# Kernel optimization log

Hardware: AMD Instinct MI355X
Metric: run time of the kernel (lower is better)

## Reference

```python
import jax, jax.numpy as jnp
import numpy as np

BLOCK_SIZE = 64
IN_CHANNELS = 1024
OUT_CHANNELS = 1024
O_NBLOCKS = OUT_CHANNELS // BLOCK_SIZE  # 16
I_NBLOCKS = IN_CHANNELS // BLOCK_SIZE   # 16
N_TOKENS = 32768


def setup_inputs() -> dict:
    key = jax.random.key(0)
    kx, kw = jax.random.split(key)
    x = jax.random.normal(kx, (N_TOKENS, IN_CHANNELS), dtype=jnp.float32)
    # xavier_uniform over the (o_nblocks, i_nblocks, block_size) tensor:
    # fan_in = i_nblocks * block_size, fan_out = block_size (last-dim convention)
    fan_in = I_NBLOCKS * BLOCK_SIZE
    fan_out = BLOCK_SIZE
    limit = float(np.sqrt(6.0 / (fan_in + fan_out)))
    w = jax.random.uniform(kw, (O_NBLOCKS, I_NBLOCKS, BLOCK_SIZE),
                           dtype=jnp.float32, minval=-limit, maxval=limit)
    return {"x": x, "w": w}


def _build_dense_weight(w):
    # w: (R, Q, bs). Dense W[r*bs+i, q*bs+j] = w[r, q, (i - j) mod bs]
    R, Q, bs = w.shape
    i = jnp.arange(bs)
    idx = (i[:, None] - i[None, :]) % bs          # (bs, bs) circulant index
    Wb = w[:, :, idx]                              # (R, Q, bs, bs)
    return Wb.transpose(0, 2, 1, 3).reshape(R * bs, Q * bs)  # (out, in)


def reference(x, w):
    W = _build_dense_weight(w)                     # (out_channels, in_channels)
    return x @ W.T                                 # F.linear, no bias
```

## Files before the change

kernel.cpp:

```cpp
#include <hip/hip_runtime.h>
#include <stdint.h>


#define NTOK 32768
#define NCH  1024
#define BK   64
#define NKT  (NCH / BK)

typedef short bf16x8 __attribute__((ext_vector_type(8)));
typedef float f32x4  __attribute__((ext_vector_type(4)));
typedef unsigned short u16x8 __attribute__((ext_vector_type(8)));

static __device__ __forceinline__ unsigned short f2bf(float f) {
    unsigned int u = __float_as_uint(f);
    u += 0x7FFFu + ((u >> 16) & 1u);
    return (unsigned short)(u >> 16);
}

#define GLOAD16(gp, lp)                                                          \
    __builtin_amdgcn_global_load_lds(                                            \
        (const __attribute__((address_space(1))) unsigned int*)(gp),             \
        (__attribute__((address_space(3))) unsigned int*)(lp), 16, 0, 0)

static __device__ __forceinline__ bf16x8 cvt8(f32x4 l, f32x4 h) {
    union { unsigned int w[4]; bf16x8 v; } u;
    asm("v_cvt_pk_bf16_f32 %0, %1, %2" : "=v"(u.w[0]) : "v"(l[0]), "v"(l[1]));
    asm("v_cvt_pk_bf16_f32 %0, %1, %2" : "=v"(u.w[1]) : "v"(l[2]), "v"(l[3]));
    asm("v_cvt_pk_bf16_f32 %0, %1, %2" : "=v"(u.w[2]) : "v"(h[0]), "v"(h[1]));
    asm("v_cvt_pk_bf16_f32 %0, %1, %2" : "=v"(u.w[3]) : "v"(h[2]), "v"(h[3]));
    return u.v;
}

__global__ void build_w_kernel(const float* __restrict__ w, unsigned short* __restrict__ Wb) {
    int i = blockIdx.x * blockDim.x + threadIdx.x;
    int o = i >> 7;
    int j = i & 127;
    int r = o >> 6;
    int q = j >> 3;
    const float* wrow = w + ((r * 16 + q) << 6);
    int k0 = j << 3;
    u16x8 v;
#pragma unroll
    for (int e = 0; e < 8; ++e) v[e] = f2bf(wrow[(o - (k0 + e)) & 63]);
    int js = (j & ~7) | ((j & 7) ^ (o & 7));
    *(u16x8*)(Wb + (((size_t)o) << 10) + (js << 3)) = v;
}

#define PHASE_BAR() __builtin_amdgcn_s_barrier()
#define VMCNT0() asm volatile("s_waitcnt vmcnt(0)" ::: "memory")
#define CFENCE() asm volatile("" ::: "memory")
#define SETPRIO(n) __builtin_amdgcn_s_setprio(n)
#define MFMA4(d, av, bv) d = __builtin_amdgcn_mfma_f32_16x16x32_bf16(av, bv, d, 0, 0, 0)
#define NOHOOK ((void)0)

#define STAGE_A(buf, tk) do {                                                    \
    const char* _s = srcA + ((tk) << 8);                                         \
    char* _d = (buf) + (wv << 10);                                               \
    GLOAD16(_s,                        _d);                                      \
    GLOAD16(_s + ((size_t)64 << 12),   _d + 8192);                               \
    GLOAD16(_s + 128,                  _d + 16384);                              \
    GLOAD16(_s + 128 + ((size_t)64 << 12), _d + 24576);                          \
} while (0)

#define STAGE_B(buf, tk) do {                                                    \
    const char* _s = srcB + ((tk) << 7);                                         \
    char* _d = (buf) + (wv << 10);                                               \
    GLOAD16(_s,                        _d);                                      \
    GLOAD16(_s + ((size_t)64 << 11),   _d + 8192);                               \
    GLOAD16(_s + ((size_t)128 << 11),  _d + 16384);                              \
    GLOAD16(_s + ((size_t)192 << 11),  _d + 24576);                              \
} while (0)

#define KSTEP(Ard, Brd, STG) do {                                                \
    STG;                                                                         \
    bf16x8 bfr[4][2];                                                            \
    _Pragma("unroll") for (int n = 0; n < 4; ++n)                                \
      _Pragma("unroll") for (int ks = 0; ks < 2; ++ks)                           \
        bfr[n][ks] = *(const bf16x8*)((Brd) + b_off[ks] + n * 2048);             \
    SETPRIO(1);                                                                  \
    _Pragma("unroll") for (int m = 0; m < 4; ++m) {                              \
        f32x4 lo0 = *(const f32x4*)((Ard) + a_rd[0][0] + m * 2048);              \
        f32x4 hi0 = *(const f32x4*)((Ard) + a_rd[0][1] + m * 2048);              \
        f32x4 lo1 = *(const f32x4*)((Ard) + a_rd[1][0] + m * 2048);              \
        f32x4 hi1 = *(const f32x4*)((Ard) + a_rd[1][1] + m * 2048);              \
        bf16x8 a0 = cvt8(lo0, hi0);                                              \
        bf16x8 a1 = cvt8(lo1, hi1);                                              \
        _Pragma("unroll") for (int n = 0; n < 4; ++n) {                          \
            MFMA4(acc[m][n], a0, bfr[n][0]);                                     \
            MFMA4(acc[m][n], a1, bfr[n][1]);                                     \
        }                                                                        \
    }                                                                            \
    SETPRIO(0);                                                                  \
    VMCNT0(); PHASE_BAR(); CFENCE();                                             \
} while (0)

__global__ void __launch_bounds__(512, 1) gemm_fused_kernel(const float* __restrict__ X,
                                                            const unsigned short* __restrict__ B,
                                                            float* __restrict__ C) {
    __shared__ __align__(16) char lds[131072];
    char* As0 = lds;
    char* As1 = lds + 32768;
    char* Bs0 = lds + 65536;
    char* Bs1 = lds + 98304;

    int tid  = threadIdx.x;
    int lane = tid & 63;
    int wv   = tid >> 6;
    int wr   = wv >> 2;
    int wc   = wv & 3;

    int cpx = gridDim.x >> 3;
    int wid = ((int)blockIdx.x & 7) * cpx + ((int)blockIdx.x >> 3);
    int tn = wid & 3, tm = wid >> 2;
    int m0 = tm * 128, n0 = tn * 256;

    const char* srcA = (const char*)X + (((size_t)(m0 + (tid >> 3))) << 12)
                     + ((((tid & 7) ^ ((tid >> 3) & 7))) << 4);

    const char* srcB = (const char*)B + (((size_t)(n0 + (tid >> 3))) << 11) + ((tid & 7) << 4);

    int r7   = lane & 7;
    int g2   = (lane >> 4) << 1;
    int abase = (wr * 64 + (lane & 15)) * 128;
    int a_rd[2][2];
#pragma unroll
    for (int ks = 0; ks < 2; ++ks)
#pragma unroll
        for (int h = 0; h < 2; ++h)
            a_rd[ks][h] = ks * 16384 + abase + (((g2 + h) ^ r7) << 4);

    int kq16 = (lane >> 4) << 4;
    int bbase = (wc * 64 + (lane & 15)) * 128;
    int b_off[2] = { bbase + ((kq16 + 0)  ^ (r7 << 4)),
                     bbase + ((kq16 + 64) ^ (r7 << 4)) };

    f32x4 acc[4][4] = {};

    STAGE_A(As0, 0); STAGE_B(Bs0, 0);
    VMCNT0(); PHASE_BAR(); CFENCE();

    for (int t = 0; t < NKT; t += 2) {
        KSTEP(As0, Bs0, { STAGE_A(As1, t + 1); STAGE_B(Bs1, t + 1); });
        if (t + 2 < NKT) {
            KSTEP(As1, Bs1, { STAGE_A(As0, t + 2); STAGE_B(Bs0, t + 2); });
        } else {
            KSTEP(As1, Bs1, NOHOOK);
        }
    }

    float* Cp = C + ((size_t)(m0 + wr * 64)) * NCH + n0 + wc * 64;
    int cc = lane & 15;
    int rr = (lane >> 4) << 2;
#pragma unroll
    for (int m = 0; m < 4; ++m)
#pragma unroll
        for (int j = 0; j < 4; ++j) {
            float* rowp = Cp + ((size_t)(m * 16 + rr + j)) * NCH;
#pragma unroll
            for (int n = 0; n < 4; ++n)
                rowp[n * 16 + cc] = acc[m][n][j];
        }
}

__global__ void naive_kernel(const float* __restrict__ x, const float* __restrict__ w,
                             float* __restrict__ out) {
    int t = blockIdx.x;
    int o = blockIdx.y * 256 + threadIdx.x;
    const float* xr = x + (size_t)t * NCH;
    int r = o >> 6, oi = o & 63;
    float s = 0.f;
    for (int q = 0; q < 16; ++q) {
        const float* wq = w + (r * 16 + q) * 64;
        const float* xq = xr + q * 64;
#pragma unroll 8
        for (int j = 0; j < 64; ++j) s += xq[j] * wq[(oi - j) & 63];
    }
    out[(size_t)t * NCH + o] = s;
}

extern "C" void kernel_launch(void* const* d_in, const int* in_sizes, int n_in,
                              void* d_out, int out_size, void* d_ws, size_t ws_size,
                              hipStream_t stream) {
    const float* x = (const float*)d_in[0];
    const float* w = (const float*)d_in[1];
    float* out = (float*)d_out;

    const size_t needW = (size_t)NCH * NCH * sizeof(unsigned short);

    if (ws_size >= needW) {
        unsigned short* Wb = (unsigned short*)d_ws;
        hipLaunchKernelGGL(build_w_kernel, dim3(NCH * 128 / 256), dim3(256), 0, stream, w, Wb);
        hipLaunchKernelGGL(gemm_fused_kernel, dim3(1024), dim3(512), 0, stream, x, Wb, out);
    } else {
        hipLaunchKernelGGL(naive_kernel, dim3(NTOK, 4), dim3(256), 0, stream, x, w, out);
    }
}
```

Before: 110.6 us.

## Shrink GEMM tile to 128x128 and pipeline A in half-tiles for occupancy

The output tile per block drops from 128x256 to 128x128, LDS use halves to 64 KB, and launch bounds now allow multiple blocks per CU with double the grid. The A tile (fp32 activations) is staged in two 16-row halves. The next half is loaded while MFMAs run on the current half, with partial vmcnt waits and extra barriers. The aim is to hide global-load latency through higher occupancy and finer-grained overlap. The cost is that each X row tile is re-read by twice as many column blocks, and there are more barriers per k-step.

```diff
diff --git a/kernel.cpp b/kernel.cpp
--- a/kernel.cpp
+++ b/kernel.cpp
@@ -4,8 +4,7 @@
 
 #define NTOK 32768
 #define NCH  1024
-#define BK   64
-#define NKT  (NCH / BK)
+#define NKT  16
 
 typedef short bf16x8 __attribute__((ext_vector_type(8)));
 typedef float f32x4  __attribute__((ext_vector_type(4)));
@@ -46,113 +45,129 @@
     *(u16x8*)(Wb + (((size_t)o) << 10) + (js << 3)) = v;
 }
 
-#define PHASE_BAR() __builtin_amdgcn_s_barrier()
-#define VMCNT0() asm volatile("s_waitcnt vmcnt(0)" ::: "memory")
+#define BAR() __builtin_amdgcn_s_barrier()
+#define LGKM0() asm volatile("s_waitcnt lgkmcnt(0)" ::: "memory")
+#define VMCNT(n) asm volatile("s_waitcnt vmcnt(" #n ")" ::: "memory")
 #define CFENCE() asm volatile("" ::: "memory")
 #define SETPRIO(n) __builtin_amdgcn_s_setprio(n)
 #define MFMA4(d, av, bv) d = __builtin_amdgcn_mfma_f32_16x16x32_bf16(av, bv, d, 0, 0, 0)
-#define NOHOOK ((void)0)
-
-#define STAGE_A(buf, tk) do {                                                    \
-    const char* _s = srcA + ((tk) << 8);                                         \
+
+#define STAGE_AH(buf, rowoff, t) do {                                            \
+    const char* _s = srcA + (((size_t)(rowoff)) << 12) + ((t) << 8);             \
     char* _d = (buf) + (wv << 10);                                               \
-    GLOAD16(_s,                        _d);                                      \
-    GLOAD16(_s + ((size_t)64 << 12),   _d + 8192);                               \
-    GLOAD16(_s + 128,                  _d + 16384);                              \
-    GLOAD16(_s + 128 + ((size_t)64 << 12), _d + 24576);                          \
-} while (0)
-
-#define STAGE_B(buf, tk) do {                                                    \
-    const char* _s = srcB + ((tk) << 7);                                         \
+    GLOAD16(_s, _d);                                                             \
+    GLOAD16(_s + ((size_t)64 << 12), _d + 8192);                                 \
+} while (0)
+
+#define STAGE_B(buf, t) do {                                                     \
+    const char* _s = srcB + ((t) << 7);                                          \
     char* _d = (buf) + (wv << 10);                                               \
-    GLOAD16(_s,                        _d);                                      \
-    GLOAD16(_s + ((size_t)64 << 11),   _d + 8192);                               \
-    GLOAD16(_s + ((size_t)128 << 11),  _d + 16384);                              \
-    GLOAD16(_s + ((size_t)192 << 11),  _d + 24576);                              \
-} while (0)
-
-#define KSTEP(Ard, Brd, STG) do {                                                \
-    STG;                                                                         \
-    bf16x8 bfr[4][2];                                                            \
+    GLOAD16(_s, _d);                                                             \
+    GLOAD16(_s + ((size_t)64 << 11), _d + 8192);                                 \
+} while (0)
+
+#define AREAD(aF, buf) do {                                                      \
+    f32x4 _l0 = *(const f32x4*)((buf) + a_rd[0][0]);                             \
+    f32x4 _h0 = *(const f32x4*)((buf) + a_rd[0][1]);                             \
+    f32x4 _l1 = *(const f32x4*)((buf) + a_rd[1][0]);                             \
+    f32x4 _h1 = *(const f32x4*)((buf) + a_rd[1][1]);                             \
+    aF[0] = cvt8(_l0, _h0);                                                      \
+    aF[1] = cvt8(_l1, _h1);                                                      \
+} while (0)
+
+#define BODY(t, Bcur, Bnxt, LAST) do {                                           \
+    bf16x8 aF0[2], aF1[2], bfr[4][2];                                            \
+    AREAD(aF0, Ah0);                                                             \
     _Pragma("unroll") for (int n = 0; n < 4; ++n)                                \
       _Pragma("unroll") for (int ks = 0; ks < 2; ++ks)                           \
-        bfr[n][ks] = *(const bf16x8*)((Brd) + b_off[ks] + n * 2048);             \
+        bfr[n][ks] = *(const bf16x8*)((Bcur) + b_off[ks] + n * 2048);            \
+    LGKM0(); BAR();                                       \
+    if (!(LAST)) { STAGE_AH(Ah0, 0, (t) + 1); STAGE_B(Bnxt, (t) + 1); }          \
     SETPRIO(1);                                                                  \
-    _Pragma("unroll") for (int m = 0; m < 4; ++m) {                              \
-        f32x4 lo0 = *(const f32x4*)((Ard) + a_rd[0][0] + m * 2048);              \
-        f32x4 hi0 = *(const f32x4*)((Ard) + a_rd[0][1] + m * 2048);              \
-        f32x4 lo1 = *(const f32x4*)((Ard) + a_rd[1][0] + m * 2048);              \
-        f32x4 hi1 = *(const f32x4*)((Ard) + a_rd[1][1] + m * 2048);              \
-        bf16x8 a0 = cvt8(lo0, hi0);                                              \
-        bf16x8 a1 = cvt8(lo1, hi1);                                              \
-        _Pragma("unroll") for (int n = 0; n < 4; ++n) {                          \
-            MFMA4(acc[m][n], a0, bfr[n][0]);                                     \
-            MFMA4(acc[m][n], a1, bfr[n][1]);                                     \
-        }                                                                        \
+    _Pragma("unroll") for (int n = 0; n < 4; ++n) {                              \
+        MFMA4(acc[0][n], aF0[0], bfr[n][0]);                                     \
+        MFMA4(acc[0][n], aF0[1], bfr[n][1]);                                     \
     }                                                                            \
     SETPRIO(0);                                                                  \
-    VMCNT0(); PHASE_BAR(); CFENCE();                                             \
-} while (0)
-
-__global__ void __launch_bounds__(512, 1) gemm_fused_kernel(const float* __restrict__ X,
+    if (LAST) { VMCNT(0); } else { VMCNT(4); }                 \
+    BAR();                                                                       \
+    AREAD(aF1, Ah1);                                                             \
+    LGKM0();                                                                     \
+    SETPRIO(1);                                                                  \
+    _Pragma("unroll") for (int n = 0; n < 4; ++n) {                              \
+        MFMA4(acc[1][n], aF1[0], bfr[n][0]);                                     \
+        MFMA4(acc[1][n], aF1[1], bfr[n][1]);                                     \
+    }                                                                            \
+    SETPRIO(0);                                                                  \
+    if (!(LAST)) {                                                               \
+        BAR();                                            \
+        STAGE_AH(Ah1, 16, (t) + 1);                                              \
+        VMCNT(2);                                     \
+        BAR(); CFENCE();                                                         \
+    }                                                                            \
+} while (0)
+
+__global__ void __launch_bounds__(512, 4) gemm_fused_kernel(const float* __restrict__ X,
                                                             const unsigned short* __restrict__ B,
                                                             float* __restrict__ C) {
-    __shared__ __align__(16) char lds[131072];
-    char* As0 = lds;
-    char* As1 = lds + 32768;
-    char* Bs0 = lds + 65536;
-    char* Bs1 = lds + 98304;
+    __shared__ __align__(16) char lds[65536];
+    char* Ah0 = lds;
+    char* Ah1 = lds + 16384;
+    char* Bs0 = lds + 32768;
+    char* Bs1 = lds + 49152;
 
     int tid  = threadIdx.x;
     int lane = tid & 63;
     int wv   = tid >> 6;
-    int wr   = wv >> 2;
-    int wc   = wv & 3;
+    int wr   = wv >> 1;
+    int wc   = wv & 1;
 
     int cpx = gridDim.x >> 3;
     int wid = ((int)blockIdx.x & 7) * cpx + ((int)blockIdx.x >> 3);
-    int tn = wid & 3, tm = wid >> 2;
-    int m0 = tm * 128, n0 = tn * 256;
-
-    const char* srcA = (const char*)X + (((size_t)(m0 + (tid >> 3))) << 12)
-                     + ((((tid & 7) ^ ((tid >> 3) & 7))) << 4);
+    int tn = wid & 7, tm = wid >> 3;
+    int m0 = tm * 128, n0 = tn * 128;
+
+    int lr0  = tid >> 4;
+    int grow = (lr0 & 15) | ((lr0 & 16) << 1);
+    int G    = tid & 15;
+    int Gl   = (G & 8) | ((G ^ (lr0 & 7)) & 7);
+    int byB  = ((Gl >> 3) << 7) | ((Gl & 3) << 5) | (((Gl >> 2) & 1) << 4);
+    const char* srcA = (const char*)X + (((size_t)(m0 + grow)) << 12) + byB;
 
     const char* srcB = (const char*)B + (((size_t)(n0 + (tid >> 3))) << 11) + ((tid & 7) << 4);
 
-    int r7   = lane & 7;
-    int g2   = (lane >> 4) << 1;
-    int abase = (wr * 64 + (lane & 15)) * 128;
+    int p = lane & 7;
+    int q = lane >> 4;
+    int abase = (wr * 16 + (lane & 15)) * 256;
     int a_rd[2][2];
 #pragma unroll
     for (int ks = 0; ks < 2; ++ks)
 #pragma unroll
         for (int h = 0; h < 2; ++h)
-            a_rd[ks][h] = ks * 16384 + abase + (((g2 + h) ^ r7) << 4);
-
-    int kq16 = (lane >> 4) << 4;
+            a_rd[ks][h] = abase + (((q | (h << 2) | (ks << 3)) ^ p) << 4);
+
+    int kq16 = q << 4;
     int bbase = (wc * 64 + (lane & 15)) * 128;
-    int b_off[2] = { bbase + ((kq16 + 0)  ^ (r7 << 4)),
-                     bbase + ((kq16 + 64) ^ (r7 << 4)) };
-
-    f32x4 acc[4][4] = {};
-
-    STAGE_A(As0, 0); STAGE_B(Bs0, 0);
-    VMCNT0(); PHASE_BAR(); CFENCE();
-
-    for (int t = 0; t < NKT; t += 2) {
-        KSTEP(As0, Bs0, { STAGE_A(As1, t + 1); STAGE_B(Bs1, t + 1); });
-        if (t + 2 < NKT) {
-            KSTEP(As1, Bs1, { STAGE_A(As0, t + 2); STAGE_B(Bs0, t + 2); });
-        } else {
-            KSTEP(As1, Bs1, NOHOOK);
-        }
+    int b_off[2] = { bbase + ((kq16 + 0)  ^ (p << 4)),
+                     bbase + ((kq16 + 64) ^ (p << 4)) };
+
+    f32x4 acc[2][4] = {};
+
+    STAGE_AH(Ah0, 0, 0); STAGE_AH(Ah1, 16, 0); STAGE_B(Bs0, 0);
+    VMCNT(0); BAR(); CFENCE();
+
+    for (int t = 0; t < NKT - 2; t += 2) {
+        BODY(t,     Bs0, Bs1, false);
+        BODY(t + 1, Bs1, Bs0, false);
     }
-
-    float* Cp = C + ((size_t)(m0 + wr * 64)) * NCH + n0 + wc * 64;
+    BODY(NKT - 2, Bs0, Bs1, false);
+    BODY(NKT - 1, Bs1, Bs0, true);
+
+    float* Cp = C + ((size_t)(m0 + wr * 32)) * NCH + n0 + wc * 64;
     int cc = lane & 15;
     int rr = (lane >> 4) << 2;
 #pragma unroll
-    for (int m = 0; m < 4; ++m)
+    for (int m = 0; m < 2; ++m)
 #pragma unroll
         for (int j = 0; j < 4; ++j) {
             float* rowp = Cp + ((size_t)(m * 16 + rr + j)) * NCH;
@@ -169,9 +184,9 @@
     const float* xr = x + (size_t)t * NCH;
     int r = o >> 6, oi = o & 63;
     float s = 0.f;
-    for (int q = 0; q < 16; ++q) {
-        const float* wq = w + (r * 16 + q) * 64;
-        const float* xq = xr + q * 64;
+    for (int qq = 0; qq < 16; ++qq) {
+        const float* wq = w + (r * 16 + qq) * 64;
+        const float* xq = xr + qq * 64;
 #pragma unroll 8
         for (int j = 0; j < 64; ++j) s += xq[j] * wq[(oi - j) & 63];
     }
@@ -190,7 +205,7 @@
     if (ws_size >= needW) {
         unsigned short* Wb = (unsigned short*)d_ws;
         hipLaunchKernelGGL(build_w_kernel, dim3(NCH * 128 / 256), dim3(256), 0, stream, w, Wb);
-        hipLaunchKernelGGL(gemm_fused_kernel, dim3(1024), dim3(512), 0, stream, x, Wb, out);
+        hipLaunchKernelGGL(gemm_fused_kernel, dim3(2048), dim3(512), 0, stream, x, Wb, out);
     } else {
         hipLaunchKernelGGL(naive_kernel, dim3(NTOK, 4), dim3(256), 0, stream, x, w, out);
     }
```

Measured after the change: 110.5 us. Within noise of the previous version (-0.1%).
